# Performance work log

Measured on AMD Instinct MI355X. Metric: run time of the kernel, lower is better.

The kernel has to match this reference:

```python
import jax, jax.numpy as jnp
import numpy as np

NUM_HEADS = 12


def setup_inputs() -> dict:
    key = jax.random.key(0)
    ks = jax.random.split(key, 5)
    B, N, C = 2, 256, 768
    x = jax.random.normal(ks[0], (B, N, C), dtype=jnp.float32)
    d = jax.random.normal(ks[1], (B, N, N, C), dtype=jnp.float32)
    w_qkv = jax.random.normal(ks[2], (3 * C, C), dtype=jnp.float32) * 0.02
    w_proj = jax.random.normal(ks[3], (C, C), dtype=jnp.float32) * 0.02
    b_proj = jnp.zeros((C,), dtype=jnp.float32)
    return {"x": x, "d": d, "w_qkv": w_qkv, "w_proj": w_proj, "b_proj": b_proj}


def reference(x, d, w_qkv, w_proj, b_proj):
    B, N, C = x.shape
    H = NUM_HEADS
    hd = C // H
    scale = hd ** -0.5
    # qkv projection (no bias, matching qkv_bias=False)
    qkv = x @ w_qkv.T                                   # [B, N, 3C]
    qkv = qkv.reshape(B, N, 3, H, hd).transpose(2, 0, 3, 1, 4)  # [3, B, H, N, hd]
    q, k, v = qkv[0] * scale, qkv[1], qkv[2]
    attn = jax.nn.softmax(jnp.einsum('bhid,bhjd->bhij', q, k), axis=-1)
    # pairwise bias per head: d -> [B, H, N, N, hd]
    dh = d.reshape(B, N, N, H, hd).transpose(0, 3, 1, 2, 4)
    # sum_j attn[...,j] * (v[j] + d[i,j]) split into the two terms
    out = jnp.einsum('bhij,bhjd->bhid', attn, v) \
        + jnp.einsum('bhij,bhijd->bhid', attn, dh)       # [B, H, N, hd]
    out = out.transpose(0, 2, 1, 3).reshape(B, N, C)
    return out @ w_proj.T + b_proj
```

## Files before the change

kernel.cpp:

```cpp
#include <hip/hip_runtime.h>

typedef __bf16 bf16_t;
typedef bf16_t bf16x8 __attribute__((ext_vector_type(8)));
typedef bf16_t bf16x4 __attribute__((ext_vector_type(4)));
typedef float f32x4 __attribute__((ext_vector_type(4)));

__device__ inline bf16x8 ld8(const float* p) {
    f32x4 a = *reinterpret_cast<const f32x4*>(p);
    f32x4 b = *reinterpret_cast<const f32x4*>(p + 4);
    bf16x8 r = { (bf16_t)a[0], (bf16_t)a[1], (bf16_t)a[2], (bf16_t)a[3],
                 (bf16_t)b[0], (bf16_t)b[1], (bf16_t)b[2], (bf16_t)b[3] };
    return r;
}
__device__ inline bf16x8 ld8(const bf16_t* p) {
    return *reinterpret_cast<const bf16x8*>(p);
}

template <typename AT, typename BT, typename OUT_T, bool HAS_BIAS>
__global__ __launch_bounds__(256) void gemm_bt(
    const AT* __restrict__ A, const BT* __restrict__ B,
    OUT_T* __restrict__ C, const float* __restrict__ bias,
    int K, int lda, int ldb, int ldc)
{
    const int l  = blockIdx.x;
    const int lp = (l & 7) * (gridDim.x >> 3) + (l >> 3);
    const int m0 = (lp & 7) * 64;
    const int n0 = (lp >> 3) * 64;

    __shared__ __align__(16) bf16_t As[64][72];
    __shared__ __align__(16) bf16_t Bs[64][72];

    const int tid  = threadIdx.x;
    const int lane = tid & 63;
    const int wave = tid >> 6;
    const int srow = tid >> 3;
    const int soff = (tid & 7) * 8;

    bf16x8 rA0, rA1, rB0, rB1;
    rA0 = ld8(&A[(long)(m0 + srow)      * lda + soff]);
    rA1 = ld8(&A[(long)(m0 + srow + 32) * lda + soff]);
    rB0 = ld8(&B[(long)(n0 + srow)      * ldb + soff]);
    rB1 = ld8(&B[(long)(n0 + srow + 32) * ldb + soff]);

    f32x4 acc[4] = {};

    for (int k0 = 0; k0 < K; k0 += 64) {
        *reinterpret_cast<bf16x8*>(&As[srow][soff])      = rA0;
        *reinterpret_cast<bf16x8*>(&As[srow + 32][soff]) = rA1;
        *reinterpret_cast<bf16x8*>(&Bs[srow][soff])      = rB0;
        *reinterpret_cast<bf16x8*>(&Bs[srow + 32][soff]) = rB1;
        __syncthreads();

        if (k0 + 64 < K) {
            rA0 = ld8(&A[(long)(m0 + srow)      * lda + k0 + 64 + soff]);
            rA1 = ld8(&A[(long)(m0 + srow + 32) * lda + k0 + 64 + soff]);
            rB0 = ld8(&B[(long)(n0 + srow)      * ldb + k0 + 64 + soff]);
            rB1 = ld8(&B[(long)(n0 + srow + 32) * ldb + k0 + 64 + soff]);
        }

#pragma unroll
        for (int ks = 0; ks < 64; ks += 32) {
            bf16x8 af = *reinterpret_cast<const bf16x8*>(&As[wave * 16 + (lane & 15)][(lane >> 4) * 8 + ks]);
#pragma unroll
            for (int nf = 0; nf < 4; ++nf) {
                bf16x8 bfr = *reinterpret_cast<const bf16x8*>(&Bs[nf * 16 + (lane & 15)][(lane >> 4) * 8 + ks]);
                acc[nf] = __builtin_amdgcn_mfma_f32_16x16x32_bf16(af, bfr, acc[nf], 0, 0, 0);
            }
        }
        __syncthreads();
    }

    const int crow0 = m0 + wave * 16 + (lane >> 4) * 4;
    const int ccol0 = n0 + (lane & 15);
#pragma unroll
    for (int nf = 0; nf < 4; ++nf) {
        const int col = ccol0 + nf * 16;
        const float bv = HAS_BIAS ? bias[col] : 0.0f;
#pragma unroll
        for (int v = 0; v < 4; ++v) {
            C[(long)(crow0 + v) * ldc + col] = (OUT_T)(acc[nf][v] + bv);
        }
    }
}

__global__ __launch_bounds__(256) void qk_softmax(
    const bf16_t* __restrict__ qkv,
    float* __restrict__ probs)
{
    const int bh = blockIdx.x;
    const int b = bh / 12, h = bh % 12;
    const int m0 = blockIdx.y * 64;
    const bf16_t* qbase = qkv + (long)b * 589824 + h * 64;
    const bf16_t* kbase = qkv + (long)b * 589824 + 768 + h * 64;

    __shared__ __align__(16) bf16_t Qs[64][72];
    __shared__ __align__(16) bf16_t Ks[256][72];

    const int t = threadIdx.x;
#pragma unroll
    for (int c = 0; c < 2; ++c) {
        const int chunk = c * 256 + t;
        const int row = chunk >> 3, off = (chunk & 7) * 8;
        *reinterpret_cast<uint4*>(&Qs[row][off]) =
            *reinterpret_cast<const uint4*>(qbase + (long)(m0 + row) * 2304 + off);
    }
#pragma unroll
    for (int c = 0; c < 8; ++c) {
        const int chunk = c * 256 + t;
        const int row = chunk >> 3, off = (chunk & 7) * 8;
        *reinterpret_cast<uint4*>(&Ks[row][off]) =
            *reinterpret_cast<const uint4*>(kbase + (long)row * 2304 + off);
    }
    __syncthreads();

    const int lane = t & 63, wave = t >> 6;
    f32x4 acc[16] = {};
#pragma unroll
    for (int ks = 0; ks < 64; ks += 32) {
        bf16x8 af = *reinterpret_cast<const bf16x8*>(&Qs[wave * 16 + (lane & 15)][(lane >> 4) * 8 + ks]);
#pragma unroll
        for (int nf = 0; nf < 16; ++nf) {
            bf16x8 bfr = *reinterpret_cast<const bf16x8*>(&Ks[nf * 16 + (lane & 15)][(lane >> 4) * 8 + ks]);
            acc[nf] = __builtin_amdgcn_mfma_f32_16x16x32_bf16(af, bfr, acc[nf], 0, 0, 0);
        }
    }

    float inv[4];
#pragma unroll
    for (int v = 0; v < 4; ++v) {
        float mm = -1e30f;
#pragma unroll
        for (int nf = 0; nf < 16; ++nf) { acc[nf][v] *= 0.125f; mm = fmaxf(mm, acc[nf][v]); }
#pragma unroll
        for (int o = 1; o < 16; o <<= 1) mm = fmaxf(mm, __shfl_xor(mm, o));
        float s = 0.0f;
#pragma unroll
        for (int nf = 0; nf < 16; ++nf) { float e = __expf(acc[nf][v] - mm); acc[nf][v] = e; s += e; }
#pragma unroll
        for (int o = 1; o < 16; o <<= 1) s += __shfl_xor(s, o);
        inv[v] = 1.0f / s;
    }

    float* prow = probs + ((long)bh * 256 + m0 + wave * 16 + (lane >> 4) * 4) * 256 + (lane & 15);
#pragma unroll
    for (int nf = 0; nf < 16; ++nf) {
#pragma unroll
        for (int v = 0; v < 4; ++v) {
            prow[(long)v * 256 + nf * 16] = acc[nf][v] * inv[v];
        }
    }
}

__global__ __launch_bounds__(256) void attnd_kernel(
    const float* __restrict__ attn,
    const bf16_t* __restrict__ qkv,
    const float* __restrict__ d,
    bf16_t* __restrict__ oh)
{
    const int bi = blockIdx.x;
    const int b  = bi >> 8;
    const int i  = bi & 255;
    const int cc = blockIdx.y;
    const int t  = threadIdx.x;
    const int lane = t & 63, wave = t >> 6;

    __shared__ float attn_s[4 * 257];
    __shared__ f32x4 partial[3][64];

#pragma unroll
    for (int q = 0; q < 4; ++q) {
        attn_s[q * 257 + t] = attn[(((long)(b * 12 + cc * 4 + q)) * 256 + i) * 256 + t];
    }
    __syncthreads();

    const int c0 = cc * 256 + lane * 4;
    const float* arow = attn_s + (lane >> 4) * 257;
    const int jb = wave * 64;
    const f32x4* dp = reinterpret_cast<const f32x4*>(d + (long)bi * 196608 + (long)jb * 768 + c0);
    const bf16_t* vp = qkv + (long)b * 589824 + (long)jb * 2304 + 1536 + c0;

    f32x4 acc = {};
#pragma unroll 8
    for (int jj = 0; jj < 64; ++jj) {
        f32x4 dv = __builtin_nontemporal_load(dp + (long)jj * 192);
        bf16x4 vv = *reinterpret_cast<const bf16x4*>(vp + (long)jj * 2304);
        float a = arow[jb + jj];
        acc[0] = fmaf(a, dv[0] + (float)vv[0], acc[0]);
        acc[1] = fmaf(a, dv[1] + (float)vv[1], acc[1]);
        acc[2] = fmaf(a, dv[2] + (float)vv[2], acc[2]);
        acc[3] = fmaf(a, dv[3] + (float)vv[3], acc[3]);
    }

    if (wave) partial[wave - 1][lane] = acc;
    __syncthreads();
    if (wave == 0) {
        acc += partial[0][lane] + partial[1][lane] + partial[2][lane];
        bf16x4 o = { (bf16_t)acc[0], (bf16_t)acc[1], (bf16_t)acc[2], (bf16_t)acc[3] };
        *reinterpret_cast<bf16x4*>(oh + (long)bi * 768 + c0) = o;
    }
}

extern "C" void kernel_launch(void* const* d_in, const int* in_sizes, int n_in,
                              void* d_out, int out_size, void* d_ws, size_t ws_size,
                              hipStream_t stream) {
    const float* x      = (const float*)d_in[0];
    const float* d      = (const float*)d_in[1];
    const float* w_qkv  = (const float*)d_in[2];
    const float* w_proj = (const float*)d_in[3];
    const float* b_proj = (const float*)d_in[4];
    float* out = (float*)d_out;

    char* ws = (char*)d_ws;
    bf16_t* qkvb  = (bf16_t*)(ws + 5505024);
    float*  probs = (float*)(ws + 7864320);
    bf16_t* oh    = (bf16_t*)(ws + 14155776);

    gemm_bt<float, float, bf16_t, false><<<288, 256, 0, stream>>>(
        x, w_qkv, qkvb, nullptr, 768, 768, 768, 2304);

    qk_softmax<<<dim3(24, 4), 256, 0, stream>>>(qkvb, probs);

    attnd_kernel<<<dim3(512, 3), 256, 0, stream>>>(probs, qkvb, d, oh);

    gemm_bt<bf16_t, float, float, true><<<96, 256, 0, stream>>>(
        oh, w_proj, out, b_proj, 768, 768, 768, 768);
}
```

Baseline: 99.98 us.

## Fuse QK scores and softmax into the attention-bias accumulation kernel

Removes the separate MFMA-based QK/softmax kernel and its fp32 probability buffer. Each block of the d-streaming kernel now computes its row's scores for four heads with scalar FMAs over K read from global memory, then runs the softmax in shared memory. This saves one launch and the write and read of the probability matrix. In exchange, each QK dot product is recomputed on CUDA cores without MFMA, and every block rereads all 256 K rows.

```diff
diff --git a/kernel.cpp b/kernel.cpp
--- a/kernel.cpp
+++ b/kernel.cpp
@@ -83,76 +83,7 @@
     }
 }
 
-__global__ __launch_bounds__(256) void qk_softmax(
-    const bf16_t* __restrict__ qkv,
-    float* __restrict__ probs)
-{
-    const int bh = blockIdx.x;
-    const int b = bh / 12, h = bh % 12;
-    const int m0 = blockIdx.y * 64;
-    const bf16_t* qbase = qkv + (long)b * 589824 + h * 64;
-    const bf16_t* kbase = qkv + (long)b * 589824 + 768 + h * 64;
-
-    __shared__ __align__(16) bf16_t Qs[64][72];
-    __shared__ __align__(16) bf16_t Ks[256][72];
-
-    const int t = threadIdx.x;
-#pragma unroll
-    for (int c = 0; c < 2; ++c) {
-        const int chunk = c * 256 + t;
-        const int row = chunk >> 3, off = (chunk & 7) * 8;
-        *reinterpret_cast<uint4*>(&Qs[row][off]) =
-            *reinterpret_cast<const uint4*>(qbase + (long)(m0 + row) * 2304 + off);
-    }
-#pragma unroll
-    for (int c = 0; c < 8; ++c) {
-        const int chunk = c * 256 + t;
-        const int row = chunk >> 3, off = (chunk & 7) * 8;
-        *reinterpret_cast<uint4*>(&Ks[row][off]) =
-            *reinterpret_cast<const uint4*>(kbase + (long)row * 2304 + off);
-    }
-    __syncthreads();
-
-    const int lane = t & 63, wave = t >> 6;
-    f32x4 acc[16] = {};
-#pragma unroll
-    for (int ks = 0; ks < 64; ks += 32) {
-        bf16x8 af = *reinterpret_cast<const bf16x8*>(&Qs[wave * 16 + (lane & 15)][(lane >> 4) * 8 + ks]);
-#pragma unroll
-        for (int nf = 0; nf < 16; ++nf) {
-            bf16x8 bfr = *reinterpret_cast<const bf16x8*>(&Ks[nf * 16 + (lane & 15)][(lane >> 4) * 8 + ks]);
-            acc[nf] = __builtin_amdgcn_mfma_f32_16x16x32_bf16(af, bfr, acc[nf], 0, 0, 0);
-        }
-    }
-
-    float inv[4];
-#pragma unroll
-    for (int v = 0; v < 4; ++v) {
-        float mm = -1e30f;
-#pragma unroll
-        for (int nf = 0; nf < 16; ++nf) { acc[nf][v] *= 0.125f; mm = fmaxf(mm, acc[nf][v]); }
-#pragma unroll
-        for (int o = 1; o < 16; o <<= 1) mm = fmaxf(mm, __shfl_xor(mm, o));
-        float s = 0.0f;
-#pragma unroll
-        for (int nf = 0; nf < 16; ++nf) { float e = __expf(acc[nf][v] - mm); acc[nf][v] = e; s += e; }
-#pragma unroll
-        for (int o = 1; o < 16; o <<= 1) s += __shfl_xor(s, o);
-        inv[v] = 1.0f / s;
-    }
-
-    float* prow = probs + ((long)bh * 256 + m0 + wave * 16 + (lane >> 4) * 4) * 256 + (lane & 15);
-#pragma unroll
-    for (int nf = 0; nf < 16; ++nf) {
-#pragma unroll
-        for (int v = 0; v < 4; ++v) {
-            prow[(long)v * 256 + nf * 16] = acc[nf][v] * inv[v];
-        }
-    }
-}
-
-__global__ __launch_bounds__(256) void attnd_kernel(
-    const float* __restrict__ attn,
+__global__ __launch_bounds__(256) void attnd_fused(
     const bf16_t* __restrict__ qkv,
     const float* __restrict__ d,
     bf16_t* __restrict__ oh)
@@ -164,17 +95,53 @@
     const int t  = threadIdx.x;
     const int lane = t & 63, wave = t >> 6;
 
-    __shared__ float attn_s[4 * 257];
+    __shared__ float qf[4][64];
+    __shared__ float attn_s[4][257];
     __shared__ f32x4 partial[3][64];
 
+    qf[t >> 6][t & 63] = (float)qkv[(long)b * 589824 + (long)i * 2304 + cc * 256 + t] * 0.125f;
+    __syncthreads();
+
+    {
+        const bf16_t* kp = qkv + (long)b * 589824 + 768 + (long)t * 2304 + cc * 256;
+        float s[4];
 #pragma unroll
-    for (int q = 0; q < 4; ++q) {
-        attn_s[q * 257 + t] = attn[(((long)(b * 12 + cc * 4 + q)) * 256 + i) * 256 + t];
+        for (int hh = 0; hh < 4; ++hh) {
+            float a = 0.0f;
+#pragma unroll
+            for (int e8 = 0; e8 < 8; ++e8) {
+                bf16x8 kv = *reinterpret_cast<const bf16x8*>(kp + hh * 64 + e8 * 8);
+#pragma unroll
+                for (int u = 0; u < 8; ++u)
+                    a = fmaf(qf[hh][e8 * 8 + u], (float)kv[u], a);
+            }
+            s[hh] = a;
+        }
+#pragma unroll
+        for (int hh = 0; hh < 4; ++hh) attn_s[hh][t] = s[hh];
+    }
+    __syncthreads();
+
+    {
+        float v0 = attn_s[wave][lane],       v1 = attn_s[wave][lane + 64],
+              v2 = attn_s[wave][lane + 128], v3 = attn_s[wave][lane + 192];
+        float m = fmaxf(fmaxf(v0, v1), fmaxf(v2, v3));
+#pragma unroll
+        for (int o = 32; o > 0; o >>= 1) m = fmaxf(m, __shfl_xor(m, o));
+        v0 = __expf(v0 - m); v1 = __expf(v1 - m); v2 = __expf(v2 - m); v3 = __expf(v3 - m);
+        float ssum = v0 + v1 + v2 + v3;
+#pragma unroll
+        for (int o = 32; o > 0; o >>= 1) ssum += __shfl_xor(ssum, o);
+        const float inv = 1.0f / ssum;
+        attn_s[wave][lane]       = v0 * inv;
+        attn_s[wave][lane + 64]  = v1 * inv;
+        attn_s[wave][lane + 128] = v2 * inv;
+        attn_s[wave][lane + 192] = v3 * inv;
     }
     __syncthreads();
 
     const int c0 = cc * 256 + lane * 4;
-    const float* arow = attn_s + (lane >> 4) * 257;
+    const float* arow = attn_s[lane >> 4];
     const int jb = wave * 64;
     const f32x4* dp = reinterpret_cast<const f32x4*>(d + (long)bi * 196608 + (long)jb * 768 + c0);
     const bf16_t* vp = qkv + (long)b * 589824 + (long)jb * 2304 + 1536 + c0;
@@ -211,16 +178,13 @@
     float* out = (float*)d_out;
 
     char* ws = (char*)d_ws;
-    bf16_t* qkvb  = (bf16_t*)(ws + 5505024);
-    float*  probs = (float*)(ws + 7864320);
-    bf16_t* oh    = (bf16_t*)(ws + 14155776);
+    bf16_t* qkvb = (bf16_t*)(ws);
+    bf16_t* oh   = (bf16_t*)(ws + 2359296);
 
     gemm_bt<float, float, bf16_t, false><<<288, 256, 0, stream>>>(
         x, w_qkv, qkvb, nullptr, 768, 768, 768, 2304);
 
-    qk_softmax<<<dim3(24, 4), 256, 0, stream>>>(qkvb, probs);
-
-    attnd_kernel<<<dim3(512, 3), 256, 0, stream>>>(probs, qkvb, d, oh);
+    attnd_fused<<<dim3(512, 3), 256, 0, stream>>>(qkvb, d, oh);
 
     gemm_bt<bf16_t, float, float, true><<<96, 256, 0, stream>>>(
         oh, w_proj, out, b_proj, 768, 768, 768, 768);
```

Measured after the change: 135.4 us. 1.35x slower.
